# Kernel tuning notes

Measured on AMD Instinct MI355X. Metric: run time of the kernel, lower is better.

## Reference

```python
import jax, jax.numpy as jnp
import numpy as np

FSIZE = 5
PAD = FSIZE // 2


def _conv(mosaick, filts):
    # mosaick [B,1,H,W], filts [f,f,K] -> responses [B,K,H,W].
    # Cross-correlation with edge-clamped boundary (Halide clamp semantics).
    x = jnp.pad(mosaick, ((0, 0), (0, 0), (PAD, PAD), (PAD, PAD)), mode='edge')
    k = jnp.transpose(filts, (2, 0, 1))[:, None, :, :]  # [K,1,f,f] OIHW
    return jax.lax.conv_general_dilated(
        x, k, window_strides=(1, 1), padding='VALID',
        dimension_numbers=('NCHW', 'OIHW', 'NCHW'))


def setup_inputs() -> dict:
    key = jax.random.key(0)
    k1, k2, k3 = jax.random.split(key, 3)
    B, H, W, K, f = 16, 512, 512, 8, FSIZE
    std = 1.0 / (f * f)  # matches normal_(0, 1/(fsize*fsize))
    return {
        'mosaick': jax.random.normal(k1, (B, 1, H, W), dtype=jnp.float32),
        'sel_filts': jax.random.normal(k2, (f, f, K), dtype=jnp.float32) * std,
        'green_filts': jax.random.normal(k3, (f, f, K), dtype=jnp.float32) * std,
    }


def reference(mosaick, sel_filts, green_filts):
    # Per-pixel soft filter selection over K candidate green-interpolation filters.
    sel = _conv(mosaick, sel_filts)      # [B,K,H,W] selection scores
    grn = _conv(mosaick, green_filts)    # [B,K,H,W] candidate green estimates
    w = jax.nn.softmax(sel, axis=1)      # softmax over filter bank
    interp = jnp.sum(w * grn, axis=1, keepdims=True)  # [B,1,H,W]
    # GRBG Bayer: green where row parity == col parity; copy known greens.
    H, W = mosaick.shape[-2], mosaick.shape[-1]
    yy = jnp.arange(H)[:, None]
    xx = jnp.arange(W)[None, :]
    is_green = (yy % 2) == (xx % 2)      # [H,W] bool
    # Output green channel only (module returns output[:, 1:2, ...]).
    return jnp.where(is_green, mosaick, interp)
```

## Files before the change

kernel.cpp:

```cpp
#include <hip/hip_runtime.h>


#define BDIM 256
#define TW 128
#define TH 8
#define LW (TW + 4)
#define LH (TH + 4)

__device__ __forceinline__ float softmax_mix(const float s[8], const float g[8]) {
    float m = s[0];
#pragma unroll
    for (int k = 1; k < 8; ++k) m = fmaxf(m, s[k]);
    float num = 0.f, den = 0.f;
#pragma unroll
    for (int k = 0; k < 8; ++k) {
        float e = __expf(s[k] - m);
        num = fmaf(e, g[k], num);
        den += e;
    }
    return num / den;
}

__global__ __launch_bounds__(BDIM) void demosaick_kernel(
    const float* __restrict__ mos,
    const float* __restrict__ sf,
    const float* __restrict__ gf,
    float* __restrict__ out,
    int H, int W)
{
    __shared__ float tile[LH * LW];

    const int b     = blockIdx.z;
    const int tileX = blockIdx.x * TW;
    const int tileY = blockIdx.y * TH;
    const float* img = mos + (size_t)b * H * W;

    for (int i = threadIdx.x; i < LH * LW; i += BDIM) {
        int r = i / LW;
        int c = i - r * LW;
        int gy = tileY - 2 + r; gy = min(max(gy, 0), H - 1);
        int gx = tileX - 2 + c; gx = min(max(gx, 0), W - 1);
        tile[i] = img[(size_t)gy * W + gx];
    }
    __syncthreads();

    const int tx = threadIdx.x & 63;
    const int ty = threadIdx.x >> 6;
    const int lx = 2 * tx + 2;
    const int ly = 2 * ty + 2;

    float sa[8], ga[8], sb[8], gb[8];
#pragma unroll
    for (int k = 0; k < 8; ++k) { sa[k] = ga[k] = sb[k] = gb[k] = 0.f; }

#pragma unroll
    for (int dy = 0; dy < 5; ++dy) {
#pragma unroll
        for (int dx = 0; dx < 5; ++dx) {
            const float va = tile[(ly + dy - 2) * LW + (lx + 1 + dx - 2)];
            const float vb = tile[(ly + 1 + dy - 2) * LW + (lx + dx - 2)];
            const float* fs = sf + (dy * 5 + dx) * 8;
            const float* fg = gf + (dy * 5 + dx) * 8;
#pragma unroll
            for (int k = 0; k < 8; ++k) {
                const float fsv = fs[k];
                const float fgv = fg[k];
                sa[k] = fmaf(va, fsv, sa[k]);
                ga[k] = fmaf(va, fgv, ga[k]);
                sb[k] = fmaf(vb, fsv, sb[k]);
                gb[k] = fmaf(vb, fgv, gb[k]);
            }
        }
    }

    const float interpA = softmax_mix(sa, ga);
    const float interpB = softmax_mix(sb, gb);

    const float green0 = tile[ly * LW + lx];
    const float green1 = tile[(ly + 1) * LW + lx + 1];

    const int y0 = tileY + 2 * ty;
    const int x0 = tileX + 2 * tx;
    float* orow0 = out + (size_t)b * H * W + (size_t)y0 * W + x0;
    float* orow1 = orow0 + W;

    *reinterpret_cast<float2*>(orow0) = make_float2(green0, interpA);
    *reinterpret_cast<float2*>(orow1) = make_float2(interpB, green1);
}

extern "C" void kernel_launch(void* const* d_in, const int* in_sizes, int n_in,
                              void* d_out, int out_size, void* d_ws, size_t ws_size,
                              hipStream_t stream) {
    const float* mos = (const float*)d_in[0];
    const float* sf  = (const float*)d_in[1];
    const float* gf  = (const float*)d_in[2];
    float* out = (float*)d_out;

    const int H = 512, W = 512;
    const int B = in_sizes[0] / (H * W);

    dim3 grid(W / TW, H / TH, B);
    dim3 block(BDIM);
    demosaick_kernel<<<grid, block, 0, stream>>>(mos, sf, gf, out, H, W);
}
```

Baseline: 97.44 us.

## Retile to 64x32 blocks with per-thread column strips and shared filter staging

Changes the tiling to 64x32 pixel tiles. Each thread owns one column and computes four interpolated pixels down that column, caching 11 vertical tile values per dx tap so shared-memory reads are reused. Both filter banks are staged interleaved in shared memory and read as float4 broadcasts instead of being loaded from global memory. Output stores become scalar and coalesced per row rather than float2, and the 64 accumulators per thread raise register pressure, which the launch bounds cap at 4 blocks.

```diff
diff --git a/kernel.cpp b/kernel.cpp
--- a/kernel.cpp
+++ b/kernel.cpp
@@ -2,90 +2,110 @@
 
 
 #define BDIM 256
-#define TW 128
-#define TH 8
-#define LW (TW + 4)
-#define LH (TH + 4)
+#define TW 64
+#define TH 32
+#define LWT (TW + 4)
+#define LHT (TH + 4)
 
-__device__ __forceinline__ float softmax_mix(const float s[8], const float g[8]) {
-    float m = s[0];
-#pragma unroll
-    for (int k = 1; k < 8; ++k) m = fmaxf(m, s[k]);
-    float num = 0.f, den = 0.f;
-#pragma unroll
-    for (int k = 0; k < 8; ++k) {
-        float e = __expf(s[k] - m);
-        num = fmaf(e, g[k], num);
-        den += e;
-    }
-    return num / den;
-}
-
-__global__ __launch_bounds__(BDIM) void demosaick_kernel(
+__global__ __launch_bounds__(BDIM, 4) void demosaick_kernel(
     const float* __restrict__ mos,
     const float* __restrict__ sf,
     const float* __restrict__ gf,
     float* __restrict__ out,
     int H, int W)
 {
-    __shared__ float tile[LH * LW];
+    __shared__ float tile[LHT * LWT];
+    __shared__ float filt[25 * 16];
 
+    const int tid   = threadIdx.x;
     const int b     = blockIdx.z;
     const int tileX = blockIdx.x * TW;
     const int tileY = blockIdx.y * TH;
     const float* img = mos + (size_t)b * H * W;
 
-    for (int i = threadIdx.x; i < LH * LW; i += BDIM) {
-        int r = i / LW;
-        int c = i - r * LW;
-        int gy = tileY - 2 + r; gy = min(max(gy, 0), H - 1);
-        int gx = tileX - 2 + c; gx = min(max(gx, 0), W - 1);
+    for (int i = tid; i < LHT * LWT; i += BDIM) {
+        int r = i / LWT;
+        int c = i - r * LWT;
+        int gy = min(max(tileY - 2 + r, 0), H - 1);
+        int gx = min(max(tileX - 2 + c, 0), W - 1);
         tile[i] = img[(size_t)gy * W + gx];
+    }
+    for (int i = tid; i < 400; i += BDIM) {
+        int tap = i >> 4;
+        int c   = i & 15;
+        filt[i] = (c < 8) ? sf[tap * 8 + c] : gf[tap * 8 + (c - 8)];
     }
     __syncthreads();
 
-    const int tx = threadIdx.x & 63;
-    const int ty = threadIdx.x >> 6;
-    const int lx = 2 * tx + 2;
-    const int ly = 2 * ty + 2;
+    const int lane = tid & 63;
+    const int g    = tid >> 6;
+    const int xc   = tileX + lane;
+    const int p    = xc & 1;
+    const int lx   = lane + 2;
+    const int y0   = tileY + g * 8;
 
-    float sa[8], ga[8], sb[8], gb[8];
+    float acc[4][16];
 #pragma unroll
-    for (int k = 0; k < 8; ++k) { sa[k] = ga[k] = sb[k] = gb[k] = 0.f; }
+    for (int r = 0; r < 4; ++r)
+#pragma unroll
+        for (int k = 0; k < 16; ++k) acc[r][k] = 0.f;
 
+    const int rowbase = g * 8 + 1 - p;
+
+    for (int dx = 0; dx < 5; ++dx) {
+        const int cx = lx + dx - 2;
+        float cache[11];
 #pragma unroll
-    for (int dy = 0; dy < 5; ++dy) {
+        for (int i = 0; i < 11; ++i)
+            cache[i] = tile[(rowbase + i) * LWT + cx];
 #pragma unroll
-        for (int dx = 0; dx < 5; ++dx) {
-            const float va = tile[(ly + dy - 2) * LW + (lx + 1 + dx - 2)];
-            const float vb = tile[(ly + 1 + dy - 2) * LW + (lx + dx - 2)];
-            const float* fs = sf + (dy * 5 + dx) * 8;
-            const float* fg = gf + (dy * 5 + dx) * 8;
+        for (int dy = 0; dy < 5; ++dy) {
+            const float4* fp = (const float4*)&filt[(dy * 5 + dx) * 16];
+            const float4 f0 = fp[0];
+            const float4 f1 = fp[1];
+            const float4 f2 = fp[2];
+            const float4 f3 = fp[3];
 #pragma unroll
-            for (int k = 0; k < 8; ++k) {
-                const float fsv = fs[k];
-                const float fgv = fg[k];
-                sa[k] = fmaf(va, fsv, sa[k]);
-                ga[k] = fmaf(va, fgv, ga[k]);
-                sb[k] = fmaf(vb, fsv, sb[k]);
-                gb[k] = fmaf(vb, fgv, gb[k]);
+            for (int r = 0; r < 4; ++r) {
+                const float v = cache[2 * r + dy];
+                acc[r][0]  = fmaf(v, f0.x, acc[r][0]);
+                acc[r][1]  = fmaf(v, f0.y, acc[r][1]);
+                acc[r][2]  = fmaf(v, f0.z, acc[r][2]);
+                acc[r][3]  = fmaf(v, f0.w, acc[r][3]);
+                acc[r][4]  = fmaf(v, f1.x, acc[r][4]);
+                acc[r][5]  = fmaf(v, f1.y, acc[r][5]);
+                acc[r][6]  = fmaf(v, f1.z, acc[r][6]);
+                acc[r][7]  = fmaf(v, f1.w, acc[r][7]);
+                acc[r][8]  = fmaf(v, f2.x, acc[r][8]);
+                acc[r][9]  = fmaf(v, f2.y, acc[r][9]);
+                acc[r][10] = fmaf(v, f2.z, acc[r][10]);
+                acc[r][11] = fmaf(v, f2.w, acc[r][11]);
+                acc[r][12] = fmaf(v, f3.x, acc[r][12]);
+                acc[r][13] = fmaf(v, f3.y, acc[r][13]);
+                acc[r][14] = fmaf(v, f3.z, acc[r][14]);
+                acc[r][15] = fmaf(v, f3.w, acc[r][15]);
             }
         }
     }
 
-    const float interpA = softmax_mix(sa, ga);
-    const float interpB = softmax_mix(sb, gb);
-
-    const float green0 = tile[ly * LW + lx];
-    const float green1 = tile[(ly + 1) * LW + lx + 1];
-
-    const int y0 = tileY + 2 * ty;
-    const int x0 = tileX + 2 * tx;
-    float* orow0 = out + (size_t)b * H * W + (size_t)y0 * W + x0;
-    float* orow1 = orow0 + W;
-
-    *reinterpret_cast<float2*>(orow0) = make_float2(green0, interpA);
-    *reinterpret_cast<float2*>(orow1) = make_float2(interpB, green1);
+    const size_t ob = (size_t)b * H * W;
+#pragma unroll
+    for (int r = 0; r < 4; ++r) {
+        float m = acc[r][0];
+#pragma unroll
+        for (int k = 1; k < 8; ++k) m = fmaxf(m, acc[r][k]);
+        float num = 0.f, den = 0.f;
+#pragma unroll
+        for (int k = 0; k < 8; ++k) {
+            float e = __expf(acc[r][k] - m);
+            num = fmaf(e, acc[r][8 + k], num);
+            den += e;
+        }
+        const float interp = num / den;
+        const float green  = tile[(g * 8 + 2 * r + p + 2) * LWT + lx];
+        out[ob + (size_t)(y0 + 2 * r + p) * W + xc]     = green;
+        out[ob + (size_t)(y0 + 2 * r + 1 - p) * W + xc] = interp;
+    }
 }
 
 extern "C" void kernel_launch(void* const* d_in, const int* in_sizes, int n_in,
```

Measured after the change: 99.99 us. 2.6% more time.

## Compute filter-bank convolutions with bf16 MFMA and shuffle-based softmax reduction

Applied to the files above, without the earlier changes.

Replaces the scalar FP32 FMA convolution with bf16 MFMA 16x16x32 instructions. The 5x5 filter taps are arranged as an A matrix and shared-memory image rows as B, so the sixteen filter outputs are computed as matrix products. The tile is stored in LDS as bf16, and interior tiles are loaded with vectorised, unclamped reads. Softmax partial sums are exchanged between lanes with cross-lane shuffles, with values packed through bf16. Precision falls to bf16 for inputs, filters, the exchanged green estimates and the num/den partial sums, which risks tolerance failures. The softmax also drops the max subtraction, so exp could overflow for large scores.

```diff
diff --git a/kernel.cpp b/kernel.cpp
--- a/kernel.cpp
+++ b/kernel.cpp
@@ -1,91 +1,147 @@
 #include <hip/hip_runtime.h>
 
 
-#define BDIM 256
-#define TW 128
-#define TH 8
-#define LW (TW + 4)
-#define LH (TH + 4)
+typedef float f32x4 __attribute__((ext_vector_type(4)));
+typedef short s16x8 __attribute__((ext_vector_type(8)));
 
-__device__ __forceinline__ float softmax_mix(const float s[8], const float g[8]) {
-    float m = s[0];
-#pragma unroll
-    for (int k = 1; k < 8; ++k) m = fmaxf(m, s[k]);
-    float num = 0.f, den = 0.f;
-#pragma unroll
-    for (int k = 0; k < 8; ++k) {
-        float e = __expf(s[k] - m);
-        num = fmaf(e, g[k], num);
-        den += e;
-    }
-    return num / den;
+#define HH 512
+#define WW 512
+#define TW 64
+#define TH 16
+#define RS 80
+#define NROW 20
+#define NEL 72
+
+__device__ __forceinline__ unsigned short bf16rne(float x) {
+    unsigned u = __float_as_uint(x);
+    u += 0x7fffu + ((u >> 16) & 1u);
+    return (unsigned short)(u >> 16);
 }
+__device__ __forceinline__ int pk2(float hi, float lo) {
+    return (int)((((unsigned)bf16rne(hi)) << 16) | (unsigned)bf16rne(lo));
+}
+__device__ __forceinline__ float hi16(int v) { return __uint_as_float(((unsigned)v) & 0xffff0000u); }
+__device__ __forceinline__ float lo16(int v) { return __uint_as_float(((unsigned)v) << 16); }
 
-__global__ __launch_bounds__(BDIM) void demosaick_kernel(
+__global__ __launch_bounds__(256) void demosaick_kernel(
     const float* __restrict__ mos,
     const float* __restrict__ sf,
     const float* __restrict__ gf,
-    float* __restrict__ out,
-    int H, int W)
+    float* __restrict__ out)
 {
-    __shared__ float tile[LH * LW];
+    __shared__ alignas(16) unsigned short tileS[NROW * RS];
 
-    const int b     = blockIdx.z;
-    const int tileX = blockIdx.x * TW;
-    const int tileY = blockIdx.y * TH;
-    const float* img = mos + (size_t)b * H * W;
+    const int tid   = threadIdx.x;
+    const int bx    = blockIdx.x;
+    const int by    = blockIdx.y;
+    const int bimg  = blockIdx.z;
+    const int tileX = bx * TW;
+    const int tileY = by * TH;
+    const float* img = mos + (size_t)bimg * HH * WW;
 
-    for (int i = threadIdx.x; i < LH * LW; i += BDIM) {
-        int r = i / LW;
-        int c = i - r * LW;
-        int gy = tileY - 2 + r; gy = min(max(gy, 0), H - 1);
-        int gx = tileX - 2 + c; gx = min(max(gx, 0), W - 1);
-        tile[i] = img[(size_t)gy * W + gx];
+    const bool interior = (bx >= 1) && (bx <= 6) && (by >= 1) && (by <= 30);
+    if (interior) {
+        if (tid < 180) {
+            int r = tid / 9, s = tid - 9 * r;
+            const float2* src = (const float2*)(img + (size_t)(tileY - 2 + r) * WW
+                                                + (tileX - 2 + 8 * s));
+            float2 v0 = src[0], v1 = src[1], v2 = src[2], v3 = src[3];
+            int4 d;
+            d.x = pk2(v0.y, v0.x);
+            d.y = pk2(v1.y, v1.x);
+            d.z = pk2(v2.y, v2.x);
+            d.w = pk2(v3.y, v3.x);
+            *(int4*)&tileS[r * RS + 8 * s] = d;
+        }
+    } else {
+        for (int i = tid; i < NROW * NEL; i += 256) {
+            int r = i / NEL, e = i - NEL * r;
+            int gy = min(max(tileY - 2 + r, 0), HH - 1);
+            int gx = min(max(tileX - 2 + e, 0), WW - 1);
+            tileS[r * RS + e] = bf16rne(img[(size_t)gy * WW + gx]);
+        }
     }
+
+    const int lane = tid & 63;
+    const int w    = tid >> 6;
+    const int ch   = lane & 15;
+    const int q    = lane >> 4;
+
+    float fv1[5], fv2[5];
+#pragma unroll
+    for (int dx = 0; dx < 5; ++dx) {
+        int t1 = (q * 5 + dx) * 8;
+        fv1[dx] = (ch < 8) ? sf[t1 + ch] : gf[t1 + ch - 8];
+        int t2 = (20 + dx) * 8;
+        fv2[dx] = (q == 0) ? ((ch < 8) ? sf[t2 + ch] : gf[t2 + ch - 8]) : 0.f;
+    }
+    s16x8 A1[2], A2[2];
+#pragma unroll
+    for (int p = 0; p < 2; ++p) {
+#pragma unroll
+        for (int j = 0; j < 8; ++j) {
+            int dx = j - p;
+            bool ok = (dx >= 0) && (dx <= 4);
+            A1[p][j] = ok ? (short)bf16rne(fv1[ok ? dx : 0]) : (short)0;
+            A2[p][j] = ok ? (short)bf16rne(fv2[ok ? dx : 0]) : (short)0;
+        }
+    }
+
     __syncthreads();
 
-    const int tx = threadIdx.x & 63;
-    const int ty = threadIdx.x >> 6;
-    const int lx = 2 * tx + 2;
-    const int ly = 2 * ty + 2;
-
-    float sa[8], ga[8], sb[8], gb[8];
-#pragma unroll
-    for (int k = 0; k < 8; ++k) { sa[k] = ga[k] = sb[k] = gb[k] = 0.f; }
+    const int* tb = (const int*)tileS;
+    float* outp = out + (size_t)bimg * HH * WW;
 
 #pragma unroll
-    for (int dy = 0; dy < 5; ++dy) {
+    for (int i = 0; i < 4; ++i) {
+        const int rloc = 4 * w + i;
+        const int p    = 1 - (i & 1);
+        const int y    = tileY + rloc;
 #pragma unroll
-        for (int dx = 0; dx < 5; ++dx) {
-            const float va = tile[(ly + dy - 2) * LW + (lx + 1 + dx - 2)];
-            const float vb = tile[(ly + 1 + dy - 2) * LW + (lx + dx - 2)];
-            const float* fs = sf + (dy * 5 + dx) * 8;
-            const float* fg = gf + (dy * 5 + dx) * 8;
-#pragma unroll
-            for (int k = 0; k < 8; ++k) {
-                const float fsv = fs[k];
-                const float fgv = fg[k];
-                sa[k] = fmaf(va, fsv, sa[k]);
-                ga[k] = fmaf(va, fgv, ga[k]);
-                sb[k] = fmaf(vb, fsv, sb[k]);
-                gb[k] = fmaf(vb, fgv, gb[k]);
+        for (int G = 0; G < 2; ++G) {
+            int bi1 = (rloc + q) * (RS / 2) + (lane & 15) + 16 * G;
+            union { int4 i; s16x8 s; } b1, b2;
+            b1.i.x = tb[bi1];     b1.i.y = tb[bi1 + 1];
+            b1.i.z = tb[bi1 + 2]; b1.i.w = tb[bi1 + 3];
+            int bi2 = (rloc + 4) * (RS / 2) + (lane & 15) + 16 * G;
+            b2.i.x = tb[bi2];     b2.i.y = tb[bi2 + 1];
+            b2.i.z = tb[bi2 + 2]; b2.i.w = tb[bi2 + 3];
+
+            f32x4 acc = __builtin_amdgcn_mfma_f32_16x16x32_bf16(
+                            A1[p], b1.s, (f32x4)(0.f), 0, 0, 0);
+            acc = __builtin_amdgcn_mfma_f32_16x16x32_bf16(
+                            A2[p], b2.s, acc, 0, 0, 0);
+
+            int d0 = pk2(acc[0], acc[1]);
+            int d1 = pk2(acc[2], acc[3]);
+            int e0 = __shfl_xor(d0, 32);
+            int e1 = __shfl_xor(d1, 32);
+            float g0 = hi16(e0), g1 = lo16(e0), g2 = hi16(e1), g3 = lo16(e1);
+
+            float x0 = __expf(acc[0]);
+            float x1 = __expf(acc[1]);
+            float x2 = __expf(acc[2]);
+            float x3 = __expf(acc[3]);
+            float den4 = (x0 + x1) + (x2 + x3);
+            float num4 = fmaf(x0, g0, fmaf(x1, g1, fmaf(x2, g2, x3 * g3)));
+
+            int nd  = pk2(num4, den4);
+            int nd2 = __shfl_xor(nd, 16);
+            float num = num4 + hi16(nd2);
+            float den = den4 + lo16(nd2);
+            float interp = num / den;
+
+            if (lane < 16) {
+                int xbase = tileX + 32 * G + 2 * lane;
+                int xg    = xbase + (1 - p);
+                float green = img[(size_t)y * WW + xg];
+                float2 st;
+                st.x = p ? green : interp;
+                st.y = p ? interp : green;
+                *(float2*)(outp + (size_t)y * WW + xbase) = st;
             }
         }
     }
-
-    const float interpA = softmax_mix(sa, ga);
-    const float interpB = softmax_mix(sb, gb);
-
-    const float green0 = tile[ly * LW + lx];
-    const float green1 = tile[(ly + 1) * LW + lx + 1];
-
-    const int y0 = tileY + 2 * ty;
-    const int x0 = tileX + 2 * tx;
-    float* orow0 = out + (size_t)b * H * W + (size_t)y0 * W + x0;
-    float* orow1 = orow0 + W;
-
-    *reinterpret_cast<float2*>(orow0) = make_float2(green0, interpA);
-    *reinterpret_cast<float2*>(orow1) = make_float2(interpB, green1);
 }
 
 extern "C" void kernel_launch(void* const* d_in, const int* in_sizes, int n_in,
@@ -96,10 +152,9 @@
     const float* gf  = (const float*)d_in[2];
     float* out = (float*)d_out;
 
-    const int H = 512, W = 512;
-    const int B = in_sizes[0] / (H * W);
+    const int B = in_sizes[0] / (HH * WW);
 
-    dim3 grid(W / TW, H / TH, B);
-    dim3 block(BDIM);
-    demosaick_kernel<<<grid, block, 0, stream>>>(mos, sf, gf, out, H, W);
+    dim3 grid(WW / TW, HH / TH, B);
+    dim3 block(256);
+    demosaick_kernel<<<grid, block, 0, stream>>>(mos, sf, gf, out);
 }
```

Result: faster. 90.06 us (-7.6%).
